# Kernel optimization log

Measured on AMD Instinct MI355X. Metric: run time of the kernel, lower is better.

Reference implementation:

```python
import jax, jax.numpy as jnp
import numpy as np

EMB = 64
HID = 1024
SEQ = 9
BATCH = 4096


def setup_inputs() -> dict:
    key = jax.random.key(0)
    ks = jax.random.split(key, 10)
    s = lambda *sh: 1.0 / np.sqrt(sh[-1])
    return {
        "observed": jax.random.normal(ks[0], (SEQ, BATCH, 2), dtype=jnp.float32),
        "W_emb": jax.random.normal(ks[1], (EMB, 2), dtype=jnp.float32) * s(2),
        "b_emb": jnp.zeros((EMB,), dtype=jnp.float32),
        "W_ih": jax.random.normal(ks[2], (4 * HID, EMB), dtype=jnp.float32) * s(EMB),
        "b_ih": jnp.zeros((4 * HID,), dtype=jnp.float32),
        "W_hh": jax.random.normal(ks[3], (4 * HID, HID), dtype=jnp.float32) * s(HID),
        "b_hh": jnp.zeros((4 * HID,), dtype=jnp.float32),
        "W_out": jax.random.normal(ks[4], (5, HID), dtype=jnp.float32) * s(HID),
        "b_out": jnp.zeros((5,), dtype=jnp.float32),
        "n_predict": 12,
    }


def _cell(x, h, c, W_ih, b_ih, W_hh, b_hh):
    # torch.nn.LSTMCell gate math, gate order i, f, g, o
    gates = x @ W_ih.T + b_ih + h @ W_hh.T + b_hh  # [B, 4H]
    i, f, g, o = jnp.split(gates, 4, axis=-1)
    c_new = jax.nn.sigmoid(f) * c + jax.nn.sigmoid(i) * jnp.tanh(g)
    h_new = jax.nn.sigmoid(o) * jnp.tanh(c_new)
    return h_new, c_new


def reference(observed, W_emb, b_emb, W_ih, b_ih, W_hh, b_hh, W_out, b_out, n_predict):
    B = observed.shape[1]
    H = W_hh.shape[1]
    h0 = jnp.zeros((B, H), dtype=observed.dtype)
    c0 = jnp.zeros((B, H), dtype=observed.dtype)

    diffs = observed[1:] - observed[:-1]  # [SEQ-1, B, 2]

    def obs_step(carry, d):
        h, c = carry
        emb = jax.nn.relu(d @ W_emb.T + b_emb)  # [B, EMB]
        h, c = _cell(emb, h, c, W_ih, b_ih, W_hh, b_hh)
        normal = h @ W_out.T + b_out  # [B, 5]
        return (h, c), normal

    (h, c), normals_obs = jax.lax.scan(obs_step, (h0, c0), diffs)
    new_vel = normals_obs[-1][:, :2]

    def pred_step(carry, _):
        h, c, nv = carry
        emb = jax.nn.relu(jax.lax.stop_gradient(nv) @ W_emb.T + b_emb)
        h, c = _cell(emb, h, c, W_ih, b_ih, W_hh, b_hh)
        normal = h @ W_out.T + b_out
        return (h, c, normal[:, :2]), normal

    (_, _, _), normals_pred = jax.lax.scan(
        pred_step, (h, c, new_vel), None, length=n_predict - 1)

    # training-mode output: stacked raw 'normal' params, shape [SEQ-1+n_predict-1, B, 5]
    return jnp.concatenate([normals_obs, normals_pred], axis=0)
```

## Files before the change

### kernel.cpp

```cpp
#include <hip/hip_runtime.h>
#include <stdint.h>
#include <stddef.h>

#define BATCH 4096
#define HID   1024
#define EMB   64
#define NKH   32
#define NSTEP 19
#define NOBS  8
#define WSL   139264

typedef _Float16 f16;
typedef _Float16 half8 __attribute__((ext_vector_type(8)));
typedef float    float4v __attribute__((ext_vector_type(4)));

__device__ __forceinline__ float sigm(float x) { return 1.f / (1.f + __expf(-x)); }
__device__ __forceinline__ float tanh_f(float x) { return 1.f - 2.f / (__expf(2.f * x) + 1.f); }

typedef const __attribute__((address_space(1))) unsigned int gau32;
typedef __attribute__((address_space(3))) unsigned int lau32;

__device__ __forceinline__ void gload16(const void* src, void* lds) {
  __builtin_amdgcn_global_load_lds((gau32*)src, (lau32*)lds, 16, 0, 0);
}

__global__ void pack_kernel(const float* __restrict__ W_ih, const float* __restrict__ b_ih,
                            const float* __restrict__ W_hh, const float* __restrict__ b_hh,
                            f16* __restrict__ Wsw, float* __restrict__ bc) {
  int gid = blockIdx.x * blockDim.x + threadIdx.x;
  int tt = gid / WSL;
  int rem = gid - tt * WSL;
  int kt = rem >> 12;
  int ni = (rem >> 9) & 7;
  int lane = (rem >> 3) & 63;
  int e = rem & 7;
  int p = tt * 128 + ni * 16 + (lane & 15);
  int g = (p >> 4) & 3;
  int u = (p >> 8) * 64 + ((p >> 6) & 3) * 16 + (p & 15);
  int orig = g * HID + u;
  int k = kt * 32 + ((lane >> 4) << 3) + e;
  float val = (k < EMB) ? W_ih[orig * EMB + k] : W_hh[orig * HID + (k - EMB)];
  Wsw[gid] = (f16)val;
  if (k == 0) bc[p] = b_ih[orig] + b_hh[orig];
}

__global__ __launch_bounds__(512, 2)
void gemm_cell_kernel(const f16* __restrict__ Xp, const f16* __restrict__ Wsw,
                      const float* __restrict__ bc,
                      f16* __restrict__ c_ws, f16* __restrict__ Xn,
                      float* __restrict__ po_ws, const float* __restrict__ W_out,
                      const float* __restrict__ obs_t, const float* __restrict__ outprev,
                      int mode, const float* __restrict__ W_emb,
                      const float* __restrict__ b_emb) {
  __shared__ f16 smem[65536];

  const int tid = threadIdx.x;
  const int lane = tid & 63;
  const int w = tid >> 6;
  const int l15 = lane & 15;
  const int quad = lane >> 4;
  const int wm = w >> 2, wn = w & 3;
  const int sh = wn >> 1, nq = wn & 1;

  const int id = blockIdx.x;
  const int x = id & 7, rr0 = id >> 3;
  const int bn = x * 2 + (rr0 & 1);
  const int bm = rr0 >> 1;
  const int slice = bn * 2 + sh;

  float4v acc[8][4];
#pragma unroll
  for (int mi = 0; mi < 8; ++mi)
#pragma unroll
    for (int ni = 0; ni < 4; ++ni) acc[mi][ni] = (float4v){0.f, 0.f, 0.f, 0.f};

  auto stage = [&](int sp) {
    const int bix = ((sp - 1) & 3) * 16384;
    const int kh = sp - 1;
#pragma unroll
    for (int i = 0; i < 2; ++i) {
      const int rtl = w * 2 + i;
      gload16(Xp + ((size_t)(bm * 16 + rtl) * NKH + kh) * 512 + lane * 8,
              smem + bix + rtl * 512);
      const int shn = w * 2 + i;
      gload16(Wsw + (size_t)(bn * 2 + (shn >> 3)) * WSL + (2 + kh) * 4096 + (shn & 7) * 512 +
                  lane * 8,
              smem + bix + 8192 + shn * 512);
    }
  };

  auto compute = [&](int s) {
    const f16* base = smem + ((s - 1) & 3) * 16384;
    half8 a[8], bq[4];
#pragma unroll
    for (int mi = 0; mi < 8; ++mi)
      a[mi] = *(const half8*)(base + (wm * 8 + mi) * 512 + lane * 8);
#pragma unroll
    for (int ni = 0; ni < 4; ++ni)
      bq[ni] = *(const half8*)(base + 8192 + (sh * 8 + nq * 4 + ni) * 512 + lane * 8);
    __builtin_amdgcn_s_setprio(1);
#pragma unroll
    for (int mi = 0; mi < 8; ++mi)
#pragma unroll
      for (int ni = 0; ni < 4; ++ni)
        acc[mi][ni] = __builtin_amdgcn_mfma_f32_16x16x32_f16(a[mi], bq[ni], acc[mi][ni], 0, 0, 0);
    __builtin_amdgcn_s_setprio(0);
  };

  {
    float d0[8], d1[8];
#pragma unroll
    for (int mi = 0; mi < 8; ++mi) {
      const int row = (bm * 16 + wm * 8 + mi) * 16 + l15;
      if (mode <= 1) {
        const float* o = obs_t + (size_t)row * 2;
        d0[mi] = o[BATCH * 2] - o[0];
        d1[mi] = o[BATCH * 2 + 1] - o[1];
      } else {
        d0[mi] = outprev[(size_t)row * 5 + 0];
        d1[mi] = outprev[(size_t)row * 5 + 1];
      }
    }
#pragma unroll
    for (int kt = 0; kt < 2; ++kt) {
      float w0[8], w1[8], be[8];
#pragma unroll
      for (int e = 0; e < 8; ++e) {
        const int j = kt * 32 + quad * 8 + e;
        w0[e] = W_emb[2 * j];
        w1[e] = W_emb[2 * j + 1];
        be[e] = b_emb[j];
      }
      half8 bfe[4];
#pragma unroll
      for (int ni = 0; ni < 4; ++ni)
        bfe[ni] = *(const half8*)(Wsw + (size_t)slice * WSL + kt * 4096 + (nq * 4 + ni) * 512 + lane * 8);
#pragma unroll
      for (int mi = 0; mi < 8; ++mi) {
        half8 ae;
#pragma unroll
        for (int e = 0; e < 8; ++e)
          ae[e] = (f16)fmaxf(d0[mi] * w0[e] + d1[mi] * w1[e] + be[e], 0.f);
#pragma unroll
        for (int ni = 0; ni < 4; ++ni)
          acc[mi][ni] = __builtin_amdgcn_mfma_f32_16x16x32_f16(ae, bfe[ni], acc[mi][ni], 0, 0, 0);
      }
    }
  }

  if (mode != 0) {
    asm volatile("s_waitcnt vmcnt(0)" ::: "memory");
    stage(1);
    stage(2);
    stage(3);
    for (int s = 1; s <= 29; ++s) {
      asm volatile("s_waitcnt vmcnt(8)" ::: "memory");
      __builtin_amdgcn_s_barrier();
      __builtin_amdgcn_sched_barrier(0);
      stage(s + 3);
      compute(s);
    }
    asm volatile("s_waitcnt vmcnt(8)" ::: "memory");
    __builtin_amdgcn_s_barrier();
    __builtin_amdgcn_sched_barrier(0);
    compute(30);
    asm volatile("s_waitcnt vmcnt(4)" ::: "memory");
    __builtin_amdgcn_s_barrier();
    __builtin_amdgcn_sched_barrier(0);
    compute(31);
    asm volatile("s_waitcnt vmcnt(0)" ::: "memory");
    __builtin_amdgcn_s_barrier();
    __builtin_amdgcn_sched_barrier(0);
    compute(32);
  }

  float bb[4];
#pragma unroll
  for (int ni = 0; ni < 4; ++ni) bb[ni] = bc[bn * 256 + wn * 64 + ni * 16 + l15];
  const int u = bn * 64 + wn * 16 + l15;
  float wo[5];
#pragma unroll
  for (int o = 0; o < 5; ++o) wo[o] = W_out[o * HID + u];

  f16* cbase = c_ws + (((size_t)(bm * 16 + bn) * 8 + w) * 64 + lane) * 32;
  half8 cv[4];
  if (mode != 0) {
#pragma unroll
    for (int q = 0; q < 4; ++q) cv[q] = *(const half8*)(cbase + q * 8);
  }

  __syncthreads();
  float* pol = (float*)smem;

#pragma unroll
  for (int mi = 0; mi < 8; ++mi) {
#pragma unroll
    for (int r = 0; r < 4; ++r) {
      const int rl = wm * 128 + mi * 16 + quad * 4 + r;
      const int row = bm * 256 + rl;
      const int ci = mi * 4 + r;
      float gi = acc[mi][0][r] + bb[0];
      float gf = acc[mi][1][r] + bb[1];
      float gg = acc[mi][2][r] + bb[2];
      float go = acc[mi][3][r] + bb[3];
      float co = (mode == 0) ? 0.f : (float)cv[ci >> 3][ci & 7];
      float cn = sigm(gf) * co + sigm(gi) * tanh_f(gg);
      cv[ci >> 3][ci & 7] = (f16)cn;
      float h = sigm(go) * tanh_f(cn);
      Xn[(((size_t)(row >> 4) * NKH + slice) * 64 + (quad * 4 + r) +
          16 * ((wn & 1) * 2 + (l15 >> 3))) * 8 + (l15 & 7)] = (f16)h;
      float pa[5];
#pragma unroll
      for (int o = 0; o < 5; ++o) pa[o] = h * wo[o];
#pragma unroll
      for (int o = 0; o < 5; ++o) {
        pa[o] += __shfl_xor(pa[o], 1, 64);
        pa[o] += __shfl_xor(pa[o], 2, 64);
        pa[o] += __shfl_xor(pa[o], 4, 64);
        pa[o] += __shfl_xor(pa[o], 8, 64);
      }
      if (l15 == 0) {
#pragma unroll
        for (int o = 0; o < 5; ++o) pol[(rl * 4 + wn) * 5 + o] = pa[o];
      }
    }
  }
#pragma unroll
  for (int q = 0; q < 4; ++q) *(half8*)(cbase + q * 8) = cv[q];

  __syncthreads();
  for (int idx = tid; idx < 1280; idx += 512) {
    const int rl = idx / 5, o = idx - rl * 5;
    float s = 0.f;
#pragma unroll
    for (int j = 0; j < 4; ++j) s += pol[(rl * 4 + j) * 5 + o];
    po_ws[((size_t)bn * BATCH + bm * 256 + rl) * 5 + o] = s;
  }
}

__global__ __launch_bounds__(256)
void reduce_kernel(const float* __restrict__ po_ws, const float* __restrict__ b_out,
                   float* __restrict__ out_t) {
  const int tid = threadIdx.x;
  const int r0 = blockIdx.x * 32;
  if (tid < 160) {
    const int rowl = tid / 5, o = tid - rowl * 5;
    const int row = r0 + rowl;
    float s = 0.f;
#pragma unroll
    for (int g = 0; g < 16; ++g) s += po_ws[((size_t)g * BATCH + row) * 5 + o];
    out_t[(size_t)row * 5 + o] = s + b_out[o];
  }
}

extern "C" void kernel_launch(void* const* d_in, const int* in_sizes, int n_in,
                              void* d_out, int out_size, void* d_ws, size_t ws_size,
                              hipStream_t stream) {
  const float* observed = (const float*)d_in[0];
  const float* W_emb = (const float*)d_in[1];
  const float* b_emb = (const float*)d_in[2];
  const float* W_ih = (const float*)d_in[3];
  const float* b_ih = (const float*)d_in[4];
  const float* W_hh = (const float*)d_in[5];
  const float* b_hh = (const float*)d_in[6];
  const float* W_out = (const float*)d_in[7];
  const float* b_out = (const float*)d_in[8];
  float* out = (float*)d_out;

  uint8_t* ws = (uint8_t*)d_ws;
  const size_t WSW_BYTES = (size_t)32 * WSL * sizeof(f16);
  const size_t XH_BYTES = (size_t)256 * NKH * 64 * 8 * sizeof(f16);
  f16* Wsw = (f16*)ws;
  float* bc = (float*)(ws + WSW_BYTES);
  f16* X0 = (f16*)(ws + WSW_BYTES + 16384);
  f16* X1 = (f16*)(ws + WSW_BYTES + 16384 + XH_BYTES);
  f16* c_ws = (f16*)(ws + WSW_BYTES + 16384 + 2 * XH_BYTES);
  float* po_ws = (float*)(ws + WSW_BYTES + 16384 + 2 * XH_BYTES + (size_t)BATCH * HID * 2);

  pack_kernel<<<(32 * WSL) / 256, 256, 0, stream>>>(W_ih, b_ih, W_hh, b_hh, Wsw, bc);

  for (int t = 0; t < NSTEP; ++t) {
    f16* Xc = (t & 1) ? X1 : X0;
    f16* Xq = (t & 1) ? X0 : X1;
    const int mode = (t == 0) ? 0 : (t < NOBS ? 1 : 2);
    gemm_cell_kernel<<<256, 512, 0, stream>>>(
        Xq, Wsw, bc, c_ws, Xc, po_ws, W_out,
        observed + (size_t)t * BATCH * 2, out + (size_t)(t - 1) * BATCH * 5,
        mode, W_emb, b_emb);
    reduce_kernel<<<BATCH / 32, 256, 0, stream>>>(po_ws, b_out, out + (size_t)t * BATCH * 5);
  }
}
```

Before: 1.136 ms.

## Replace direct-to-LDS 4-stage pipeline with register-staged double buffer

Swaps the global_load_lds four-buffer prefetch pipeline for register-staged loads written to LDS through a two-buffer ping-pong, which halves the shared memory footprint. A-fragments are now read from LDS per mi row inside the MFMA loop instead of all up front, lowering register pressure. The aim is higher occupancy or a simpler schedule, at the cost of extra VGPRs for the staging registers, extra ds_write instructions, and shallower prefetch depth that could expose global latency.

```diff
diff --git a/kernel.cpp b/kernel.cpp
--- a/kernel.cpp
+++ b/kernel.cpp
@@ -16,13 +16,6 @@
 
 __device__ __forceinline__ float sigm(float x) { return 1.f / (1.f + __expf(-x)); }
 __device__ __forceinline__ float tanh_f(float x) { return 1.f - 2.f / (__expf(2.f * x) + 1.f); }
-
-typedef const __attribute__((address_space(1))) unsigned int gau32;
-typedef __attribute__((address_space(3))) unsigned int lau32;
-
-__device__ __forceinline__ void gload16(const void* src, void* lds) {
-  __builtin_amdgcn_global_load_lds((gau32*)src, (lau32*)lds, 16, 0, 0);
-}
 
 __global__ void pack_kernel(const float* __restrict__ W_ih, const float* __restrict__ b_ih,
                             const float* __restrict__ W_hh, const float* __restrict__ b_hh,
@@ -52,7 +45,7 @@
                       const float* __restrict__ obs_t, const float* __restrict__ outprev,
                       int mode, const float* __restrict__ W_emb,
                       const float* __restrict__ b_emb) {
-  __shared__ f16 smem[65536];
+  __shared__ f16 smem[32768];
 
   const int tid = threadIdx.x;
   const int lane = tid & 63;
@@ -74,38 +67,40 @@
 #pragma unroll
     for (int ni = 0; ni < 4; ++ni) acc[mi][ni] = (float4v){0.f, 0.f, 0.f, 0.f};
 
-  auto stage = [&](int sp) {
-    const int bix = ((sp - 1) & 3) * 16384;
-    const int kh = sp - 1;
-#pragma unroll
-    for (int i = 0; i < 2; ++i) {
-      const int rtl = w * 2 + i;
-      gload16(Xp + ((size_t)(bm * 16 + rtl) * NKH + kh) * 512 + lane * 8,
-              smem + bix + rtl * 512);
-      const int shn = w * 2 + i;
-      gload16(Wsw + (size_t)(bn * 2 + (shn >> 3)) * WSL + (2 + kh) * 4096 + (shn & 7) * 512 +
-                  lane * 8,
-              smem + bix + 8192 + shn * 512);
-    }
+  half8 R[4];
+
+  auto gload = [&](int kh) {
+    R[0] = *(const half8*)(Xp + ((size_t)(bm * 16 + w * 2 + 0) * NKH + kh) * 512 + lane * 8);
+    R[1] = *(const half8*)(Xp + ((size_t)(bm * 16 + w * 2 + 1) * NKH + kh) * 512 + lane * 8);
+    R[2] = *(const half8*)(Wsw + (size_t)(bn * 2 + ((w * 2 + 0) >> 3)) * WSL +
+                           (size_t)(2 + kh) * 4096 + ((w * 2 + 0) & 7) * 512 + lane * 8);
+    R[3] = *(const half8*)(Wsw + (size_t)(bn * 2 + ((w * 2 + 1) >> 3)) * WSL +
+                           (size_t)(2 + kh) * 4096 + ((w * 2 + 1) & 7) * 512 + lane * 8);
   };
-
-  auto compute = [&](int s) {
-    const f16* base = smem + ((s - 1) & 3) * 16384;
-    half8 a[8], bq[4];
-#pragma unroll
-    for (int mi = 0; mi < 8; ++mi)
-      a[mi] = *(const half8*)(base + (wm * 8 + mi) * 512 + lane * 8);
+  auto dswr = [&](int p2) {
+    f16* buf = smem + p2 * 16384;
+    *(half8*)(buf + (w * 2 + 0) * 512 + lane * 8) = R[0];
+    *(half8*)(buf + (w * 2 + 1) * 512 + lane * 8) = R[1];
+    *(half8*)(buf + 8192 + (w * 2 + 0) * 512 + lane * 8) = R[2];
+    *(half8*)(buf + 8192 + (w * 2 + 1) * 512 + lane * 8) = R[3];
+  };
+  auto compute = [&](const f16* base) {
+    half8 bq[4];
 #pragma unroll
     for (int ni = 0; ni < 4; ++ni)
       bq[ni] = *(const half8*)(base + 8192 + (sh * 8 + nq * 4 + ni) * 512 + lane * 8);
     __builtin_amdgcn_s_setprio(1);
 #pragma unroll
-    for (int mi = 0; mi < 8; ++mi)
+    for (int mi = 0; mi < 8; ++mi) {
+      half8 am = *(const half8*)(base + (wm * 8 + mi) * 512 + lane * 8);
 #pragma unroll
       for (int ni = 0; ni < 4; ++ni)
-        acc[mi][ni] = __builtin_amdgcn_mfma_f32_16x16x32_f16(a[mi], bq[ni], acc[mi][ni], 0, 0, 0);
+        acc[mi][ni] = __builtin_amdgcn_mfma_f32_16x16x32_f16(am, bq[ni], acc[mi][ni], 0, 0, 0);
+    }
     __builtin_amdgcn_s_setprio(0);
   };
+
+  if (mode != 0) gload(0);
 
   {
     float d0[8], d1[8];
@@ -149,29 +144,19 @@
   }
 
   if (mode != 0) {
-    asm volatile("s_waitcnt vmcnt(0)" ::: "memory");
-    stage(1);
-    stage(2);
-    stage(3);
-    for (int s = 1; s <= 29; ++s) {
-      asm volatile("s_waitcnt vmcnt(8)" ::: "memory");
+    dswr(0);
+    gload(1);
+    asm volatile("s_waitcnt lgkmcnt(0)" ::: "memory");
+    __builtin_amdgcn_sched_barrier(0);
+    __builtin_amdgcn_s_barrier();
+    for (int s = 1; s <= 32; ++s) {
+      if (s < 32) dswr(s & 1);
+      if (s < 31) gload(s + 1);
+      compute(smem + ((s - 1) & 1) * 16384);
+      asm volatile("s_waitcnt lgkmcnt(0)" ::: "memory");
+      __builtin_amdgcn_sched_barrier(0);
       __builtin_amdgcn_s_barrier();
-      __builtin_amdgcn_sched_barrier(0);
-      stage(s + 3);
-      compute(s);
-    }
-    asm volatile("s_waitcnt vmcnt(8)" ::: "memory");
-    __builtin_amdgcn_s_barrier();
-    __builtin_amdgcn_sched_barrier(0);
-    compute(30);
-    asm volatile("s_waitcnt vmcnt(4)" ::: "memory");
-    __builtin_amdgcn_s_barrier();
-    __builtin_amdgcn_sched_barrier(0);
-    compute(31);
-    asm volatile("s_waitcnt vmcnt(0)" ::: "memory");
-    __builtin_amdgcn_s_barrier();
-    __builtin_amdgcn_sched_barrier(0);
-    compute(32);
+    }
   }
 
   float bb[4];
```

Measured after the change: 1.173 ms. 1.03x slower.
